# Kernel tuning notes

Hardware: AMD Instinct MI355X
Metric: run time of the kernel (lower is better)

## Reference

```python
import jax, jax.numpy as jnp
import numpy as np

NEG_INF = -jnp.inf


def setup_inputs() -> dict:
    B, T, E, H = 16, 1024, 1024, 1024  # batch, seq, embed_dim, head_dim (T <= H required by original buffer slicing)
    key = jax.random.key(0)
    k1, k2, k3, k4, k5, k6 = jax.random.split(key, 6)
    return {
        "key": jax.random.normal(k1, (B, T, E), dtype=jnp.float32),
        "query": jax.random.normal(k2, (B, T, E), dtype=jnp.float32),
        "value": jax.random.normal(k3, (B, T, E), dtype=jnp.float32),
        "padding_mask": jnp.zeros((B, 1, T), dtype=jnp.int32),
        # nn.Linear(embed_dim, head_dim, bias=False) weights: [head_dim, embed_dim]
        "Wk": jax.random.normal(k4, (H, E), dtype=jnp.float32) * (E ** -0.5),
        "Wq": jax.random.normal(k5, (H, E), dtype=jnp.float32) * (E ** -0.5),
        "Wv": jax.random.normal(k6, (H, E), dtype=jnp.float32) * (E ** -0.5),
    }


def reference(key, query, value, padding_mask, Wk, Wq, Wv):
    # key/query/value: [B, T, E]; W*: [H, E]
    B, T, E = key.shape
    k = jnp.einsum("bte,he->bth", key, Wk)
    q = jnp.einsum("bte,he->bth", query, Wq)
    v = jnp.einsum("bte,he->bth", value, Wv)
    # NOTE: original scales by d_k = key.size(-1) = embed_dim, not head_dim
    scale = 1.0 / jnp.sqrt(jnp.float32(E))
    qk = jnp.einsum("bth,bsh->bts", q, k) * scale  # [B, T, T]
    # causal buffer is tril(ones, diagonal=1): position i can attend to j <= i+1
    causal = jnp.tril(jnp.ones((T, T), dtype=jnp.float32), k=1)
    qk = jnp.where(causal == 0, NEG_INF, qk)
    qk = jnp.where(padding_mask == 1, NEG_INF, qk)  # padding_mask broadcasts [B,1,T] -> [B,T,T]
    p = jax.nn.softmax(qk, axis=-1)
    attn = jnp.einsum("bts,bsh->bth", p, v)  # dropout is identity in eval mode
    return attn
```

## Files before the change

kernel.cpp:

```cpp
#include <hip/hip_runtime.h>
#include <hip/hip_bf16.h>
#include <stdint.h>

typedef __bf16 bf16;
typedef __attribute__((ext_vector_type(8))) __bf16 bf16x8;
typedef __attribute__((ext_vector_type(4))) __bf16 bf16x4;
typedef __attribute__((ext_vector_type(4))) float  f32x4;

static __device__ __forceinline__ void gll16(const void* g, void* lds_base) {
  __builtin_amdgcn_global_load_lds((__attribute__((address_space(1))) void*)g,
                                   (__attribute__((address_space(3))) void*)lds_base,
                                   16, 0, 0);
}

#define BARR  __builtin_amdgcn_s_barrier()
#define VMW(N) asm volatile("s_waitcnt vmcnt(" #N ")" ::: "memory")
#define LGKM0 asm volatile("s_waitcnt lgkmcnt(0)" ::: "memory")
#define SB0   __builtin_amdgcn_sched_barrier(0)

template <int VARIANT>
__global__ __launch_bounds__(512, 2) void gemm8(const bf16* __restrict__ a0,
                                                const bf16* __restrict__ a1,
                                                const bf16* __restrict__ b0,
                                                const bf16* __restrict__ b1,
                                                bf16* __restrict__ c0,
                                                bf16* __restrict__ c1,
                                                float* __restrict__ Cf,
                                                const int* __restrict__ pad) {
  constexpr int TM = (VARIANT == 0) ? 256 : 128;
  constexpr int ABYTES = TM * 64;
  constexpr int AROUNDS = ABYTES / 8192;
  constexpr int FI = TM / 64;
  extern __shared__ char smem[];
  char* ldsA = smem;
  char* ldsB = smem + 2 * ABYTES;

  const int tid = threadIdx.x;
  const int lane = tid & 63, wave = tid >> 6;
  const int lo = lane & 15, hi = lane >> 4;
  const int wmi = wave >> 2, wni = wave & 3;
  const int swz = ((lo >> 1) & 3) << 4;

  const int nwg = gridDim.x;
  const int id = (blockIdx.x % 8) * (nwg >> 3) + blockIdx.x / 8;

  int row0, col0, nt, batch = 0, trans = 0;
  const bf16 *Ap, *Bp;
  bf16* Cb;
  if (VARIANT == 0) {
    const int seg = id >> 8, idl = id & 255;
    row0 = (idl >> 2) * 256; col0 = (idl & 3) * 256; nt = 32;
    trans = seg;
    const bf16* As = seg ? a1 : a0;
    const bf16* Bs = seg ? b1 : b0;
    Cb = seg ? c1 : c0;
    Ap = As + (size_t)row0 * 1024;
    Bp = Bs + (size_t)col0 * 1024;
  } else {
    batch = id >> 5;
    const int it = (id >> 2) & 7, jt = id & 3;
    row0 = it * 128; col0 = jt * 256;
    nt = (VARIANT == 3) ? min(32, 4 * it + 5) : 32;
    if (VARIANT == 2 && 2 * jt >= it + 2) {
      bf16* Sb = c0 + ((size_t)batch << 20);
      bf16x8 z = {};
#pragma unroll
      for (int q = 0; q < (TM * 256) / (512 * 8); ++q) {
        const int off = (q * 512 + tid) * 8;
        *(bf16x8*)(Sb + (size_t)(row0 + (off >> 8)) * 1024 + col0 + (off & 255)) = z;
      }
      return;
    }
    Ap = a0 + ((size_t)batch << 20) + (size_t)row0 * 1024;
    Bp = b0 + ((size_t)batch << 20) + (size_t)col0 * 1024;
    Cb = c0;
  }
  const int ntm1 = nt - 1;

  auto stgA = [&](int tidx, int slot) {
    const int tc = tidx > ntm1 ? ntm1 : tidx;
#pragma unroll
    for (int r = 0; r < AROUNDS; ++r) {
      const int x  = (r * 512 + tid) * 16;
      const int xs = x ^ (((x >> 7) & 3) << 4);
      gll16((const char*)Ap + (size_t)(xs >> 6) * 2048 + (size_t)tc * 64 + (xs & 63),
            ldsA + slot * ABYTES + r * 8192 + wave * 1024);
    }
  };
  auto stgB = [&](int tidx, int slot) {
    const int tc = tidx > ntm1 ? ntm1 : tidx;
#pragma unroll
    for (int r = 0; r < 2; ++r) {
      const int x  = (r * 512 + tid) * 16;
      const int xs = x ^ (((x >> 7) & 3) << 4);
      gll16((const char*)Bp + (size_t)(xs >> 6) * 2048 + (size_t)tc * 64 + (xs & 63),
            ldsB + slot * 16384 + r * 8192 + wave * 1024);
    }
  };

  f32x4 acc[2 * FI][4] = {};
  bf16x8 af[FI], bfr[4];

  auto rdA = [&](int mh, int slot) {
#pragma unroll
    for (int i = 0; i < FI; ++i) {
      const int row = wmi * (TM / 2) + mh * (TM / 4) + i * 16 + lo;
      af[i] = *(const bf16x8*)(ldsA + slot * ABYTES + ((row * 64 + hi * 16) ^ swz));
    }
  };
  auto rdB = [&](int slot) {
#pragma unroll
    for (int n = 0; n < 4; ++n) {
      const int row = wni * 64 + n * 16 + lo;
      bfr[n] = *(const bf16x8*)(ldsB + slot * 16384 + ((row * 64 + hi * 16) ^ swz));
    }
  };
  auto mmaQ = [&](int mh) {
    __builtin_amdgcn_s_setprio(1);
#pragma unroll
    for (int i = 0; i < FI; ++i)
#pragma unroll
      for (int n = 0; n < 4; ++n)
        acc[mh * FI + i][n] = __builtin_amdgcn_mfma_f32_16x16x32_bf16(
            af[i], bfr[n], acc[mh * FI + i][n], 0, 0, 0);
    __builtin_amdgcn_s_setprio(0);
  };

  stgB(0, 0);
  stgA(0, 0);
  stgB(1, 1);
  VMW(2);
  BARR;

#pragma unroll 2
  for (int u = 0; u < nt; ++u) {
    const int cur = u & 1;
    rdA(0, cur);
    rdB(cur);
    stgA(u + 1, cur ^ 1);
    BARR; LGKM0; SB0;
    mmaQ(0);
    BARR;
    rdA(1, cur);
    stgB(u + 2, cur);
    BARR; LGKM0; SB0;
    mmaQ(1);
    VMW(2);
    BARR;
  }

  if (VARIANT == 0) {
    if (!trans) {
#pragma unroll
      for (int m = 0; m < 2 * FI; ++m)
#pragma unroll
        for (int n = 0; n < 4; ++n) {
          const int c = col0 + wni * 64 + n * 16 + lo;
          const int rbase = row0 + wmi * (TM / 2) + m * 16 + hi * 4;
#pragma unroll
          for (int j = 0; j < 4; ++j)
            Cb[(size_t)(rbase + j) * 1024 + c] = (bf16)acc[m][n][j];
        }
    } else {
#pragma unroll
      for (int m = 0; m < 2 * FI; ++m)
#pragma unroll
        for (int n = 0; n < 4; ++n) {
          const int r = row0 + wmi * (TM / 2) + m * 16 + hi * 4;
          const int c = col0 + wni * 64 + n * 16 + lo;
          const int bb = r >> 10, tt = r & 1023;
          bf16x4 h = { (bf16)acc[m][n][0], (bf16)acc[m][n][1],
                       (bf16)acc[m][n][2], (bf16)acc[m][n][3] };
          *(bf16x4*)(Cb + ((size_t)bb << 20) + ((size_t)c << 10) + tt) = h;
        }
    }
  } else if (VARIANT == 2) {
    const float NINF = -__builtin_inff();
#pragma unroll
    for (int n = 0; n < 4; ++n) {
      const int s = col0 + wni * 64 + n * 16 + lo;
      const int pd = pad[(batch << 10) + s];
#pragma unroll
      for (int m = 0; m < 2 * FI; ++m) {
        const int tbase = row0 + wmi * (TM / 2) + m * 16 + hi * 4;
#pragma unroll
        for (int j = 0; j < 4; ++j) {
          float v = acc[m][n][j] * 0.03125f;
          if (s > tbase + j + 1) v = 0.f;
          else if (pd != 0) v = NINF;
          Cb[((size_t)batch << 20) + (size_t)(tbase + j) * 1024 + s] = (bf16)v;
        }
      }
    }
  } else {
#pragma unroll
    for (int m = 0; m < 2 * FI; ++m)
#pragma unroll
      for (int n = 0; n < 4; ++n) {
        const int h2 = col0 + wni * 64 + n * 16 + lo;
        const int tbase = row0 + wmi * (TM / 2) + m * 16 + hi * 4;
#pragma unroll
        for (int j = 0; j < 4; ++j)
          Cf[((size_t)batch << 20) + (size_t)(tbase + j) * 1024 + h2] = acc[m][n][j];
      }
  }
  asm volatile("s_waitcnt vmcnt(0)" ::: "memory");
}

__global__ __launch_bounds__(256) void cvt3_kernel(const float* __restrict__ s0,
                                                   const float* __restrict__ s1,
                                                   const float* __restrict__ s2,
                                                   bf16* __restrict__ d0,
                                                   bf16* __restrict__ d1,
                                                   bf16* __restrict__ d2) {
  const int seg = blockIdx.x >> 13, blk = blockIdx.x & 8191;
  const float* src = seg == 0 ? s0 : (seg == 1 ? s1 : s2);
  bf16* dst = seg == 0 ? d0 : (seg == 1 ? d1 : d2);
  const int i = (blk * 256 + threadIdx.x) * 8;
  const f32x4 a = *(const f32x4*)(src + i);
  const f32x4 b = *(const f32x4*)(src + i + 4);
  bf16x8 o = { (bf16)a[0], (bf16)a[1], (bf16)a[2], (bf16)a[3],
               (bf16)b[0], (bf16)b[1], (bf16)b[2], (bf16)b[3] };
  *(bf16x8*)(dst + i) = o;
}

__global__ __launch_bounds__(256) void cvtWT_kernel(const float* __restrict__ Wq,
                                                    const float* __restrict__ Wk,
                                                    const float* __restrict__ Wv,
                                                    bf16* __restrict__ WqT,
                                                    bf16* __restrict__ WkT,
                                                    bf16* __restrict__ Wvb) {
  const int t = threadIdx.x;
  if (blockIdx.x >= 512) {
    const int i = ((blockIdx.x - 512) * 256 + t) * 8;
    const f32x4 a = *(const f32x4*)(Wv + i);
    const f32x4 b = *(const f32x4*)(Wv + i + 4);
    bf16x8 o = { (bf16)a[0], (bf16)a[1], (bf16)a[2], (bf16)a[3],
                 (bf16)b[0], (bf16)b[1], (bf16)b[2], (bf16)b[3] };
    *(bf16x8*)(Wvb + i) = o;
    return;
  }
  const int m = blockIdx.x >> 8;
  const float* src = m ? Wk : Wq;
  bf16* dst = m ? WkT : WqT;
  const int tile = blockIdx.x & 255;
  const int tr = (tile >> 4) * 64, tc = (tile & 15) * 64;
  __shared__ bf16 s[64][72];
#pragma unroll
  for (int it = 0; it < 4; ++it) {
    const int row = it * 16 + (t >> 4), col = (t & 15) * 4;
    const f32x4 v = *(const f32x4*)(src + (size_t)(tr + row) * 1024 + tc + col);
#pragma unroll
    for (int j = 0; j < 4; ++j) s[col + j][row] = (bf16)v[j];
  }
  __syncthreads();
  const int c = t >> 2, rb = (t & 3) * 16;
  bf16* d = dst + (size_t)(tc + c) * 1024 + tr + rb;
  *(bf16x8*)(d)     = *(const bf16x8*)&s[c][rb];
  *(bf16x8*)(d + 8) = *(const bf16x8*)&s[c][rb + 8];
}

__global__ __launch_bounds__(256) void softmax_kernel(bf16* __restrict__ S) {
  const int row  = blockIdx.x * 4 + (threadIdx.x >> 6);
  const int lane = threadIdx.x & 63;
  const int t = row & 1023;
  const int w = min(1024, t + 2);
  const bool act = lane * 16 < w;
  bf16* r = S + (size_t)row * 1024 + lane * 16;
  bf16x8 v0 = {}, v1 = {};
  float f[16];
#pragma unroll
  for (int j = 0; j < 16; ++j) f[j] = -1e30f;
  if (act) {
    v0 = *(const bf16x8*)r;
    v1 = *(const bf16x8*)(r + 8);
#pragma unroll
    for (int j = 0; j < 16; ++j)
      if (lane * 16 + j < w) f[j] = (float)(j < 8 ? v0[j] : v1[j - 8]);
  }
  float m = f[0];
#pragma unroll
  for (int j = 1; j < 16; ++j) m = fmaxf(m, f[j]);
#pragma unroll
  for (int o = 32; o; o >>= 1) m = fmaxf(m, __shfl_xor(m, o, 64));
  float sum = 0.f;
  float e[16];
#pragma unroll
  for (int j = 0; j < 16; ++j) { e[j] = __expf(f[j] - m); sum += e[j]; }
#pragma unroll
  for (int o = 32; o; o >>= 1) sum += __shfl_xor(sum, o, 64);
  const float inv = 1.0f / sum;
  if (act) {
#pragma unroll
    for (int j = 0; j < 8; ++j) {
      v0[j] = (bf16)(lane * 16 + j < w ? e[j] * inv : 0.f);
      v1[j] = (bf16)(lane * 16 + 8 + j < w ? e[8 + j] * inv : 0.f);
    }
    *(bf16x8*)r = v0;
    *(bf16x8*)(r + 8) = v1;
  }
}

extern "C" void kernel_launch(void* const* d_in, const int* in_sizes, int n_in,
                              void* d_out, int out_size, void* d_ws, size_t ws_size,
                              hipStream_t stream) {
  const float* key   = (const float*)d_in[0];
  const float* query = (const float*)d_in[1];
  const float* value = (const float*)d_in[2];
  const int*   pad   = (const int*)d_in[3];
  const float* Wk    = (const float*)d_in[4];
  const float* Wq    = (const float*)d_in[5];
  const float* Wv    = (const float*)d_in[6];
  float* out = (float*)d_out;

  bf16* WqT = (bf16*)d_ws;
  bf16* WkT = WqT + (1 << 20);
  bf16* Wvb = WkT + (1 << 20);
  bf16* P   = Wvb + (1 << 20);
  bf16* Y   = P   + (1 << 20);
  bf16* vT  = Y   + (16 << 20);
  bf16* S   = vT  + (16 << 20);
  bf16* Xq  = S;
  bf16* Xk  = (bf16*)d_out;
  bf16* Xv  = Xk + (16 << 20);

  hipFuncSetAttribute(reinterpret_cast<const void*>(&gemm8<0>),
                      hipFuncAttributeMaxDynamicSharedMemorySize, 65536);
  hipFuncSetAttribute(reinterpret_cast<const void*>(&gemm8<2>),
                      hipFuncAttributeMaxDynamicSharedMemorySize, 49152);
  hipFuncSetAttribute(reinterpret_cast<const void*>(&gemm8<3>),
                      hipFuncAttributeMaxDynamicSharedMemorySize, 49152);

  cvtWT_kernel<<<1024, 256, 0, stream>>>(Wq, Wk, Wv, WqT, WkT, Wvb);
  gemm8<0><<<16, 512, 65536, stream>>>(WkT, nullptr, WqT, nullptr,
                                       P, nullptr, nullptr, nullptr);
  cvt3_kernel<<<24576, 256, 0, stream>>>(query, key, value, Xq, Xk, Xv);

  gemm8<0><<<512, 512, 65536, stream>>>(Xq, Xv, P, Wvb, Y, vT, nullptr, nullptr);

  gemm8<2><<<512, 512, 49152, stream>>>(Y, nullptr, Xk, nullptr,
                                        S, nullptr, nullptr, pad);
  softmax_kernel<<<4096, 256, 0, stream>>>(S);
  gemm8<3><<<512, 512, 49152, stream>>>(S, nullptr, vT, nullptr,
                                        nullptr, nullptr, out, nullptr);
}
```

Measured before the change: 240.5 us.

## Add dedicated projection GEMM kernel with K=128 tiles and quadrant-wise pipeline

Replaces the generic gemm8<0> launch for the Q/V projection with a new proj8 kernel. It uses 128-wide K tiles in 128 KB of LDS, an XOR swizzle over eight rows, and a finer schedule that splits each tile into quadrants, interleaving global-to-LDS loads with MFMA groups. The goal is fewer barriers per unit of work and better overlap of loads with math in the largest GEMM. The larger LDS footprint may cut occupancy to one block per CU despite the launch bounds asking for two.

```diff
diff --git a/kernel.cpp b/kernel.cpp
--- a/kernel.cpp
+++ b/kernel.cpp
@@ -15,8 +15,146 @@
 
 #define BARR  __builtin_amdgcn_s_barrier()
 #define VMW(N) asm volatile("s_waitcnt vmcnt(" #N ")" ::: "memory")
-#define LGKM0 asm volatile("s_waitcnt lgkmcnt(0)" ::: "memory")
-#define SB0   __builtin_amdgcn_sched_barrier(0)
+#define LGKM0 do { asm volatile("s_waitcnt lgkmcnt(0)" ::: "memory");          \
+                   __builtin_amdgcn_sched_barrier(0); } while (0)
+
+__global__ __launch_bounds__(512, 2) void proj8(const bf16* __restrict__ a0,
+                                                const bf16* __restrict__ a1,
+                                                const bf16* __restrict__ b0,
+                                                const bf16* __restrict__ b1,
+                                                bf16* __restrict__ c0,
+                                                bf16* __restrict__ c1) {
+  extern __shared__ char smem[];
+  char* ldsA = smem;
+  char* ldsB = smem + 65536;
+
+  const int tid = threadIdx.x;
+  const int lane = tid & 63, wave = tid >> 6;
+  const int lo = lane & 15, hi = lane >> 4;
+  const int wmi = wave >> 2, wni = wave & 3;
+  const int swz = (lo & 7) << 4;
+
+  const int nwg = gridDim.x;
+  const int id = (blockIdx.x % 8) * (nwg >> 3) + blockIdx.x / 8;
+  const int seg = id >> 8, idl = id & 255;
+  const int row0 = (idl >> 2) * 256, col0 = (idl & 3) * 256;
+  const bf16* Ap = (seg ? a1 : a0) + (size_t)row0 * 1024;
+  const bf16* Bp = (seg ? b1 : b0) + (size_t)col0 * 1024;
+  bf16* Cb = seg ? c1 : c0;
+
+  const char* aSrc[2];
+  const char* bSrc[2];
+  int ldsOff[2];
+#pragma unroll
+  for (int rr = 0; rr < 2; ++rr) {
+    const int x = rr * 8192 + tid * 16;
+    const int lr = x >> 7;
+    const int colx = (x & 127) ^ ((lr & 7) << 4);
+    aSrc[rr] = (const char*)Ap + (size_t)(((lr >> 6) << 7) | (lr & 63)) * 2048 + colx;
+    bSrc[rr] = (const char*)Bp + (size_t)(((lr >> 5) << 6) | (lr & 31)) * 2048 + colx;
+    ldsOff[rr] = rr * 8192 + wave * 1024;
+  }
+  auto stA = [&](int h, int buf, int t) {
+    const int tc = t > 15 ? 15 : t;
+#pragma unroll
+    for (int rr = 0; rr < 2; ++rr)
+      gll16(aSrc[rr] + h * 131072 + tc * 128,
+            ldsA + buf * 32768 + h * 16384 + ldsOff[rr]);
+  };
+  auto stB = [&](int h, int buf, int t) {
+    const int tc = t > 15 ? 15 : t;
+#pragma unroll
+    for (int rr = 0; rr < 2; ++rr)
+      gll16(bSrc[rr] + h * 65536 + tc * 128,
+            ldsB + buf * 32768 + h * 16384 + ldsOff[rr]);
+  };
+
+  f32x4 acc[8][4] = {};
+  bf16x8 af[4][2], bq0[2][2], bq1[2][2];
+
+  auto rdA = [&](int mq, int buf) {
+#pragma unroll
+    for (int i = 0; i < 4; ++i) {
+      const int lr = wmi * 64 + i * 16 + lo;
+#pragma unroll
+      for (int kh = 0; kh < 2; ++kh)
+        af[i][kh] = *(const bf16x8*)(ldsA + buf * 32768 + mq * 16384 +
+                                     lr * 128 + ((kh * 64 + hi * 16) ^ swz));
+    }
+  };
+  auto rdB = [&](bf16x8 bq[2][2], int nq, int buf) {
+#pragma unroll
+    for (int n = 0; n < 2; ++n) {
+      const int lr = wni * 32 + n * 16 + lo;
+#pragma unroll
+      for (int kh = 0; kh < 2; ++kh)
+        bq[n][kh] = *(const bf16x8*)(ldsB + buf * 32768 + nq * 16384 +
+                                     lr * 128 + ((kh * 64 + hi * 16) ^ swz));
+    }
+  };
+  auto mma = [&](bf16x8 bq[2][2], int mq, int nq) {
+    __builtin_amdgcn_s_setprio(1);
+#pragma unroll
+    for (int i = 0; i < 4; ++i)
+#pragma unroll
+      for (int n = 0; n < 2; ++n)
+#pragma unroll
+        for (int kh = 0; kh < 2; ++kh)
+          acc[mq * 4 + i][nq * 2 + n] = __builtin_amdgcn_mfma_f32_16x16x32_bf16(
+              af[i][kh], bq[n][kh], acc[mq * 4 + i][nq * 2 + n], 0, 0, 0);
+    __builtin_amdgcn_s_setprio(0);
+  };
+
+  stA(0, 0, 0); stB(1, 0, 0); stA(1, 0, 0); stB(0, 0, 0);
+  stA(0, 1, 1); stB(1, 1, 1); stA(1, 1, 1);
+  VMW(6); BARR;
+
+  for (int j = 0; j < 8; ++j) {
+    const int t1 = 2 * j + 1, t2 = 2 * j + 2, t3 = 2 * j + 3;
+    rdA(0, 0); rdB(bq0, 0, 0); stB(0, 1, t1);
+    BARR; LGKM0; mma(bq0, 0, 0); BARR;
+    rdB(bq1, 1, 0); stA(0, 0, t2);
+    BARR; LGKM0; mma(bq1, 0, 1); BARR;
+    rdA(1, 0); stB(1, 0, t2);
+    BARR; LGKM0; mma(bq1, 1, 1); BARR;
+    stA(1, 0, t2);
+    BARR; LGKM0; mma(bq0, 1, 0); VMW(6); BARR;
+    rdA(0, 1); rdB(bq0, 0, 1); stB(0, 0, t2);
+    BARR; LGKM0; mma(bq0, 0, 0); BARR;
+    rdB(bq1, 1, 1); stA(0, 1, t3);
+    BARR; LGKM0; mma(bq1, 0, 1); BARR;
+    rdA(1, 1); stB(1, 1, t3);
+    BARR; LGKM0; mma(bq1, 1, 1); BARR;
+    stA(1, 1, t3);
+    BARR; LGKM0; mma(bq0, 1, 0); VMW(6); BARR;
+  }
+
+  if (!seg) {
+#pragma unroll
+    for (int m = 0; m < 8; ++m)
+#pragma unroll
+      for (int n = 0; n < 4; ++n) {
+        const int c = col0 + wni * 64 + n * 16 + lo;
+        const int rbase = row0 + wmi * 128 + m * 16 + hi * 4;
+#pragma unroll
+        for (int j = 0; j < 4; ++j)
+          Cb[(size_t)(rbase + j) * 1024 + c] = (bf16)acc[m][n][j];
+      }
+  } else {
+#pragma unroll
+    for (int m = 0; m < 8; ++m)
+#pragma unroll
+      for (int n = 0; n < 4; ++n) {
+        const int r = row0 + wmi * 128 + m * 16 + hi * 4;
+        const int c = col0 + wni * 64 + n * 16 + lo;
+        const int bb = r >> 10, tt = r & 1023;
+        bf16x4 h = { (bf16)acc[m][n][0], (bf16)acc[m][n][1],
+                     (bf16)acc[m][n][2], (bf16)acc[m][n][3] };
+        *(bf16x4*)(Cb + ((size_t)bb << 20) + ((size_t)c << 10) + tt) = h;
+      }
+  }
+  asm volatile("s_waitcnt vmcnt(0)" ::: "memory");
+}
 
 template <int VARIANT>
 __global__ __launch_bounds__(512, 2) void gemm8(const bf16* __restrict__ a0,
@@ -44,18 +182,15 @@
   const int nwg = gridDim.x;
   const int id = (blockIdx.x % 8) * (nwg >> 3) + blockIdx.x / 8;
 
-  int row0, col0, nt, batch = 0, trans = 0;
+  int row0, col0, nt, batch = 0;
   const bf16 *Ap, *Bp;
   bf16* Cb;
   if (VARIANT == 0) {
-    const int seg = id >> 8, idl = id & 255;
+    const int idl = id & 255;
     row0 = (idl >> 2) * 256; col0 = (idl & 3) * 256; nt = 32;
-    trans = seg;
-    const bf16* As = seg ? a1 : a0;
-    const bf16* Bs = seg ? b1 : b0;
-    Cb = seg ? c1 : c0;
-    Ap = As + (size_t)row0 * 1024;
-    Bp = Bs + (size_t)col0 * 1024;
+    Ap = a0 + (size_t)row0 * 1024;
+    Bp = b0 + (size_t)col0 * 1024;
+    Cb = c0;
   } else {
     batch = id >> 5;
     const int it = (id >> 2) & 7, jt = id & 3;
@@ -138,42 +273,28 @@
     rdA(0, cur);
     rdB(cur);
     stgA(u + 1, cur ^ 1);
-    BARR; LGKM0; SB0;
+    BARR; LGKM0;
     mmaQ(0);
     BARR;
     rdA(1, cur);
     stgB(u + 2, cur);
-    BARR; LGKM0; SB0;
+    BARR; LGKM0;
     mmaQ(1);
     VMW(2);
     BARR;
   }
 
   if (VARIANT == 0) {
-    if (!trans) {
-#pragma unroll
-      for (int m = 0; m < 2 * FI; ++m)
-#pragma unroll
-        for (int n = 0; n < 4; ++n) {
-          const int c = col0 + wni * 64 + n * 16 + lo;
-          const int rbase = row0 + wmi * (TM / 2) + m * 16 + hi * 4;
-#pragma unroll
-          for (int j = 0; j < 4; ++j)
-            Cb[(size_t)(rbase + j) * 1024 + c] = (bf16)acc[m][n][j];
-        }
-    } else {
-#pragma unroll
-      for (int m = 0; m < 2 * FI; ++m)
-#pragma unroll
-        for (int n = 0; n < 4; ++n) {
-          const int r = row0 + wmi * (TM / 2) + m * 16 + hi * 4;
-          const int c = col0 + wni * 64 + n * 16 + lo;
-          const int bb = r >> 10, tt = r & 1023;
-          bf16x4 h = { (bf16)acc[m][n][0], (bf16)acc[m][n][1],
-                       (bf16)acc[m][n][2], (bf16)acc[m][n][3] };
-          *(bf16x4*)(Cb + ((size_t)bb << 20) + ((size_t)c << 10) + tt) = h;
-        }
-    }
+#pragma unroll
+    for (int m = 0; m < 2 * FI; ++m)
+#pragma unroll
+      for (int n = 0; n < 4; ++n) {
+        const int c = col0 + wni * 64 + n * 16 + lo;
+        const int rbase = row0 + wmi * (TM / 2) + m * 16 + hi * 4;
+#pragma unroll
+        for (int j = 0; j < 4; ++j)
+          Cb[(size_t)(rbase + j) * 1024 + c] = (bf16)acc[m][n][j];
+      }
   } else if (VARIANT == 2) {
     const float NINF = -__builtin_inff();
 #pragma unroll
@@ -324,6 +445,8 @@
   bf16* Xk  = (bf16*)d_out;
   bf16* Xv  = Xk + (16 << 20);
 
+  hipFuncSetAttribute(reinterpret_cast<const void*>(&proj8),
+                      hipFuncAttributeMaxDynamicSharedMemorySize, 131072);
   hipFuncSetAttribute(reinterpret_cast<const void*>(&gemm8<0>),
                       hipFuncAttributeMaxDynamicSharedMemorySize, 65536);
   hipFuncSetAttribute(reinterpret_cast<const void*>(&gemm8<2>),
@@ -336,7 +459,7 @@
                                        P, nullptr, nullptr, nullptr);
   cvt3_kernel<<<24576, 256, 0, stream>>>(query, key, value, Xq, Xk, Xv);
 
-  gemm8<0><<<512, 512, 65536, stream>>>(Xq, Xv, P, Wvb, Y, vT, nullptr, nullptr);
+  proj8<<<512, 512, 131072, stream>>>(Xq, Xv, P, Wvb, Y, vT);
 
   gemm8<2><<<512, 512, 49152, stream>>>(Y, nullptr, Xk, nullptr,
                                         S, nullptr, nullptr, pad);
```

After: 234.5 us. 1.03x faster.
